# Optimization experiments

Hardware: AMD Instinct MI355X
Metric: run time of the kernel (lower is better)

The kernel has to match this reference:

```python
import jax, jax.numpy as jnp
import numpy as np

SHARPNESS = 2


def setup_inputs() -> dict:
    key = jax.random.key(0)
    k1, k2, k3 = jax.random.split(key, 3)
    x = jax.random.normal(k1, (16, 256, 48, 48), dtype=jnp.float32)
    # 1x1 conv == per-pixel linear: weight (out_c, in_c), bias (out_c,)
    W = jax.random.normal(k2, (256, 256), dtype=jnp.float32) * 0.0625
    bias = jax.random.normal(k3, (256,), dtype=jnp.float32) * 0.01
    return {"x": x, "W": W, "bias": bias}


def reference(x, W, bias):
    b, c, h, w = x.shape
    hw = h * w
    # sample-wide L2 norm over the full (c*h*w) vector (faithful to source)
    xn = jnp.linalg.norm(x.reshape(b, -1), axis=1).reshape(b, 1, 1)
    # NOTE: raw reshapes of the (b,c,h,w)-contiguous tensor, NOT transposes
    x1 = x.reshape(b, hw, c) / xn
    x2 = x.reshape(b, c, hw) / xn
    cos = jnp.einsum('bnc,bcm->bnm', x1, x2)          # (b, hw, hw)
    s = jnp.maximum(cos, 0.0) ** SHARPNESS            # relu^sharpness
    # transform block: 1x1 conv
    tr = jnp.einsum('oc,bchw->bohw', W, x) + bias[None, :, None, None]
    tr = tr.reshape(b, hw, c)                         # raw reshape, as in source
    y = jnp.einsum('bnm,bmc->bnc', s, tr)             # (b, hw, c)
    return y.reshape(b, c, h, w)
```

## Files before the change

### kernel.cpp

```cpp
#include <hip/hip_runtime.h>

#define NB 16
#define NC 256
#define HW 2304
#define CHW 589824

typedef __attribute__((ext_vector_type(8))) short bf16x8;
typedef __attribute__((ext_vector_type(16))) float f32x16;

union BF8 { bf16x8 v; unsigned short u[8]; unsigned d[4]; };

__device__ inline unsigned short f2bf(float f) {
  unsigned u = __builtin_bit_cast(unsigned, f);
  u += 0x7fffu + ((u >> 16) & 1u);
  return (unsigned short)(u >> 16);
}

__device__ inline unsigned f2bf2(float lo, float hi) {
  unsigned r;
  asm("v_cvt_pk_bf16_f32 %0, %1, %2" : "=v"(r) : "v"(lo), "v"(hi));
  return r;
}

__global__ __launch_bounds__(256) void prep_kernel(const float* __restrict__ x,
                                                   const float* __restrict__ W,
                                                   unsigned short* __restrict__ wp,
                                                   unsigned short* __restrict__ xtp,
                                                   double* __restrict__ partials) {
  __shared__ __align__(16) char smem[33344];
  const int bid = blockIdx.x;
  const int tid = threadIdx.x;

  if (bid < 8) {
    const int rt = bid;
    float* tile = (float*)smem;
    const float4* src = (const float4*)(W + (size_t)rt * 32 * 256);
    #pragma unroll
    for (int it = 0; it < 8; ++it) {
      const int i = tid + 256 * it;
      float4 v = src[i];
      const int fi = 4 * i, row = fi >> 8, col = fi & 255;
      *(float4*)&tile[row * 260 + col] = v;
    }
    __syncthreads();
    const int w = tid >> 6, l = tid & 63, l31 = l & 31, h = l >> 5;
    unsigned short* dst = wp + (size_t)rt * 8192;
    #pragma unroll
    for (int ff = 0; ff < 4; ++ff) {
      const int f = 4 * w + ff;
      const float* rp = &tile[l31 * 260 + 16 * f + 8 * h];
      const float4 r0 = *(const float4*)rp;
      const float4 r1 = *(const float4*)(rp + 4);
      BF8 o;
      o.d[0] = f2bf2(r0.x, r0.y);
      o.d[1] = f2bf2(r0.z, r0.w);
      o.d[2] = f2bf2(r1.x, r1.y);
      o.d[3] = f2bf2(r1.z, r1.w);
      *(bf16x8*)(dst + (((size_t)f) * 64 + l) * 8) = o.v;
    }
  } else {
    const int e = bid - 8;
    const int mt = e % 36, kt = (e / 36) % 4, b = e / 144;
    const int m0 = mt * 64, k0 = kt * 64;
    float* tile = (float*)smem;
    double* red = (double*)(smem + 17408);
    const float* xb = x + (size_t)b * CHW;
    double ss = 0.0;
    #pragma unroll
    for (int it = 0; it < 4; ++it) {
      const int i = tid + 256 * it;
      const int row = i >> 4, c4 = (i & 15) * 4;
      float4 v = *(const float4*)(xb + (size_t)(k0 + row) * HW + m0 + c4);
      *(float4*)&tile[row * 68 + c4] = v;
      ss += (double)v.x * v.x + (double)v.y * v.y + (double)v.z * v.z + (double)v.w * v.w;
    }
    #pragma unroll
    for (int off = 32; off > 0; off >>= 1) ss += __shfl_down(ss, off, 64);
    const int w = tid >> 6, l = tid & 63;
    if (l == 0) red[w] = ss;
    __syncthreads();
    if (tid == 0) partials[b * 144 + kt * 36 + mt] = red[0] + red[1] + red[2] + red[3];
    const int l31 = l & 31, h = l >> 5;
    unsigned short* dst = xtp + (size_t)b * CHW;
    #pragma unroll
    for (int pp = 0; pp < 2; ++pp) {
      const int p = 2 * w + pp, mbl = p >> 2, fl = p & 3;
      BF8 o;
      #pragma unroll
      for (int jj = 0; jj < 4; ++jj) {
        const float e0 = tile[(16 * fl + 8 * h + 2 * jj) * 68 + 32 * mbl + l31];
        const float e1 = tile[(16 * fl + 8 * h + 2 * jj + 1) * 68 + 32 * mbl + l31];
        o.d[jj] = f2bf2(e0, e1);
      }
      const int mb = 2 * mt + mbl, f = 4 * kt + fl;
      *(bf16x8*)(dst + (((size_t)mb * 16 + f) * 64 + l) * 8) = o.v;
    }
  }
}

__global__ __launch_bounds__(512, 1) void conv2_kernel(const unsigned short* __restrict__ wp,
                                                       const float* __restrict__ bias,
                                                       const unsigned short* __restrict__ xtp,
                                                       unsigned short* __restrict__ trp,
                                                       const double* __restrict__ partials,
                                                       float* __restrict__ inv_xn2) {
  const int bid = blockIdx.x;
  if (bid == 128) {
    const int t = threadIdx.x;
    if (t >= 256) return;
    const int b = t >> 4, i0 = t & 15;
    double v = 0.0;
    for (int i = i0; i < 144; i += 16) v += partials[b * 144 + i];
    v += __shfl_down(v, 8, 64);
    v += __shfl_down(v, 4, 64);
    v += __shfl_down(v, 2, 64);
    v += __shfl_down(v, 1, 64);
    if (i0 == 0) inv_xn2[b] = (float)(1.0 / v);
    return;
  }
  const int xcd = bid & 7, q = bid >> 3;
  const int b = xcd + 8 * (q & 1);
  const int rt = q >> 1;
  const int tid = threadIdx.x, w = tid >> 6, l = tid & 63, l31 = l & 31, h = l >> 5;
  const unsigned short* xb = xtp + (size_t)b * CHW;

  __shared__ unsigned short tile[32 * 2312];

  bf16x8 af[16];
  #pragma unroll
  for (int f = 0; f < 16; ++f)
    af[f] = *(const bf16x8*)(wp + (((size_t)rt * 16 + f) * 64 + l) * 8);
  float bcol[16];
  #pragma unroll
  for (int reg = 0; reg < 16; ++reg) {
    const int rowl = (reg & 3) + 8 * (reg >> 2) + 4 * h;
    bcol[reg] = bias[32 * rt + rowl];
  }

  for (int i = 0; i < 9; ++i) {
    const int mb = 9 * w + i;
    f32x16 acc;
    #pragma unroll
    for (int r = 0; r < 16; ++r) acc[r] = 0.f;
    #pragma unroll
    for (int f = 0; f < 16; ++f) {
      bf16x8 bv = *(const bf16x8*)(xb + (((size_t)mb * 16 + f) * 64 + l) * 8);
      acc = __builtin_amdgcn_mfma_f32_32x32x16_bf16(af[f], bv, acc, 0, 0, 0);
    }
    #pragma unroll
    for (int p = 0; p < 8; ++p) {
      const int r0 = 2 * p, r1 = 2 * p + 1;
      const int rowl = (r0 & 3) + 8 * (r0 >> 2) + 4 * h;
      const unsigned pk = f2bf2(acc[r0] + bcol[r0], acc[r1] + bcol[r1]);
      tile[rowl * 2312 + mb * 32 + l31] = (unsigned short)pk;
      tile[(rowl + 1) * 2312 + mb * 32 + l31] = (unsigned short)(pk >> 16);
    }
  }
  __syncthreads();

  unsigned short* tb = trp + (size_t)b * CHW;
  for (int si = 0; si < 18; ++si) {
    const int id = 18 * w + si;
    const int kfi = id >> 3, cb8 = id & 7;
    const int mbase = 288 * rt + 16 * kfi;
    const int mb2 = mbase >> 6, kf = (mbase >> 4) & 3;
    BF8 o;
    #pragma unroll
    for (int j = 0; j < 8; ++j) {
      const int m = mbase + 8 * h + j;
      const int a = m / 9, s = m - 9 * a;
      o.u[j] = tile[(a - 32 * rt) * 2312 + 256 * s + 32 * cb8 + l31];
    }
    *(bf16x8*)(tb + (size_t)mb2 * 16384 + (((size_t)cb8 * 4 + kf) * 64 + l) * 8) = o.v;
  }
}

#define CHUNK_BODY(CH, CUR, NXT)                                                                   \
  {                                                                                                \
    const int ch_ = (CH);                                                                          \
    const int pb_ = ch_ & 1;                                                                       \
    f32x16 s0, s1;                                                                                 \
    _Pragma("unroll")                                                                              \
    for (int i = 0; i < 16; ++i) { s0[i] = 0.f; s1[i] = 0.f; }                                     \
    _Pragma("unroll")                                                                              \
    for (int f = 0; f < 16; ++f) {                                                                 \
      bf16x8 a0 = *(const bf16x8*)(Af + f * 512 + lane * 8);                                       \
      bf16x8 a1 = *(const bf16x8*)(Af + (16 + f) * 512 + lane * 8);                                \
      s0 = __builtin_amdgcn_mfma_f32_32x32x16_bf16(a0, CUR[f], s0, 0, 0, 0);                       \
      s1 = __builtin_amdgcn_mfma_f32_32x32x16_bf16(a1, CUR[f], s1, 0, 0, 0);                       \
    }                                                                                              \
    bf16x8 bt0[8], bt1[8];                                                                         \
    _Pragma("unroll")                                                                              \
    for (int kk = 0; kk < 8; ++kk) {                                                               \
      const size_t mb_ = 2 * ch_ + (kk >> 2);                                                      \
      bt0[kk] = *(const bf16x8*)(ttb + mb_ * 16384 + ((size_t)((2 * c) * 4 + (kk & 3))) * 512 + lane * 8);     \
      bt1[kk] = *(const bf16x8*)(ttb + mb_ * 16384 + ((size_t)((2 * c + 1) * 4 + (kk & 3))) * 512 + lane * 8); \
    }                                                                                              \
    _Pragma("unroll")                                                                              \
    for (int reg = 0; reg < 16; ++reg) {                                                           \
      const int rowp = (reg & 3) + 8 * (reg >> 2) + 4 * h;                                         \
      float v0 = fmaxf(s0[reg] * inv2, 0.f); v0 *= v0;                                             \
      float v1 = fmaxf(s1[reg] * inv2, 0.f); v1 *= v1;                                             \
      Pl[pb_][rowp][32 * c + l31] = f2bf(v0);                                                      \
      Pl[pb_][32 + rowp][32 * c + l31] = f2bf(v1);                                                 \
    }                                                                                              \
    const int chn_ = (ch_ < 17) ? ch_ + 1 : 17;                                                    \
    const unsigned short* bpn_ = xtb + (size_t)((4 * chn_ + c) * 16) * 512 + lane * 8;             \
    _Pragma("unroll")                                                                              \
    for (int f = 0; f < 16; ++f) NXT[f] = *(const bf16x8*)(bpn_ + f * 512);                        \
    __syncthreads();                                                                               \
    _Pragma("unroll")                                                                              \
    for (int kk = 0; kk < 8; ++kk) {                                                               \
      bf16x8 pf0 = *(const bf16x8*)&Pl[pb_][l31][16 * kk + 8 * h];                                 \
      bf16x8 pf1 = *(const bf16x8*)&Pl[pb_][32 + l31][16 * kk + 8 * h];                            \
      yacc[0][0] = __builtin_amdgcn_mfma_f32_32x32x16_bf16(pf0, bt0[kk], yacc[0][0], 0, 0, 0);     \
      yacc[1][0] = __builtin_amdgcn_mfma_f32_32x32x16_bf16(pf1, bt0[kk], yacc[1][0], 0, 0, 0);     \
      yacc[0][1] = __builtin_amdgcn_mfma_f32_32x32x16_bf16(pf0, bt1[kk], yacc[0][1], 0, 0, 0);     \
      yacc[1][1] = __builtin_amdgcn_mfma_f32_32x32x16_bf16(pf1, bt1[kk], yacc[1][1], 0, 0, 0);     \
    }                                                                                              \
  }

__global__ __launch_bounds__(256, 2) void fused_kernel(const float* __restrict__ x,
                                                       const unsigned short* __restrict__ xtp,
                                                       const unsigned short* __restrict__ trp,
                                                       const float* __restrict__ inv_xn2,
                                                       float* __restrict__ out) {
  const int bid = blockIdx.x;
  const int xcd = bid & 7, j = bid >> 3;
  const int hi = (j >= 36) ? 1 : 0;
  const int b = xcd + 8 * hi;
  const int nt = j - 36 * hi;
  const float* xsrc = x + (size_t)b * CHW;
  const unsigned short* xtb = xtp + (size_t)b * CHW;
  const unsigned short* ttb = trp + (size_t)b * CHW;
  float* ob = out + (size_t)b * CHW;
  const float inv2 = inv_xn2[b];

  const int tid = threadIdx.x;
  const int c = tid >> 6, lane = tid & 63;
  const int l31 = lane & 31, h = lane >> 5;

  __shared__ unsigned short Af[16384];
  __shared__ unsigned short Pl[2][64][136];

  {
    #pragma unroll
    for (int it = 0; it < 8; ++it) {
      const int idx = tid + 256 * it;
      const int f = idx >> 6, l = idx & 63;
      const int ll31 = l & 31, hh = l >> 5;
      const float* sp = xsrc + (size_t)(64 * nt + 32 * (f >> 4) + ll31) * 256 + 16 * (f & 15) + 8 * hh;
      const float4 r0 = *(const float4*)sp;
      const float4 r1 = *(const float4*)(sp + 4);
      BF8 o;
      o.d[0] = f2bf2(r0.x, r0.y);
      o.d[1] = f2bf2(r0.z, r0.w);
      o.d[2] = f2bf2(r1.x, r1.y);
      o.d[3] = f2bf2(r1.z, r1.w);
      *(bf16x8*)(Af + (size_t)f * 512 + (size_t)l * 8) = o.v;
    }
  }

  bf16x8 bva[16], bvb[16];
  {
    const unsigned short* bp0 = xtb + (size_t)(c * 16) * 512 + lane * 8;
    #pragma unroll
    for (int f = 0; f < 16; ++f) bva[f] = *(const bf16x8*)(bp0 + f * 512);
  }
  __syncthreads();

  f32x16 yacc[2][2];
  #pragma unroll
  for (int nh = 0; nh < 2; ++nh)
    #pragma unroll
    for (int cb = 0; cb < 2; ++cb)
      #pragma unroll
      for (int i = 0; i < 16; ++i) yacc[nh][cb][i] = 0.f;

  for (int ci = 0; ci < 9; ++ci) {
    CHUNK_BODY(2 * ci, bva, bvb)
    CHUNK_BODY(2 * ci + 1, bvb, bva)
  }

  #pragma unroll
  for (int nh = 0; nh < 2; ++nh)
    #pragma unroll
    for (int cb = 0; cb < 2; ++cb) {
      const int col = 64 * c + 32 * cb + l31;
      #pragma unroll
      for (int reg = 0; reg < 16; ++reg) {
        const int rowp = (reg & 3) + 8 * (reg >> 2) + 4 * h;
        ob[(size_t)(64 * nt + 32 * nh + rowp) * NC + col] = yacc[nh][cb][reg];
      }
    }
}

extern "C" void kernel_launch(void* const* d_in, const int* in_sizes, int n_in,
                              void* d_out, int out_size, void* d_ws, size_t ws_size,
                              hipStream_t stream) {
  const float* x    = (const float*)d_in[0];
  const float* W    = (const float*)d_in[1];
  const float* bias = (const float*)d_in[2];
  float* out = (float*)d_out;

  const size_t SZ = (size_t)NB * CHW * sizeof(unsigned short);
  double* partials       = (double*)d_ws;
  float* inv_xn2         = (float*)((char*)d_ws + 24576);
  unsigned short* wp     = (unsigned short*)((char*)d_ws + 32768);
  unsigned short* xtp    = (unsigned short*)((char*)d_ws + 163840 + SZ);
  unsigned short* trp    = (unsigned short*)((char*)d_ws + 163840 + 3 * SZ);

  prep_kernel<<<2312, 256, 0, stream>>>(x, W, wp, xtp, partials);
  conv2_kernel<<<129, 512, 0, stream>>>(wp, bias, xtp, trp, partials, inv_xn2);
  fused_kernel<<<576, 256, 0, stream>>>(x, xtp, trp, inv_xn2, out);
}
```

Before: 232.8 us.

## Split conv kernel into 1025 small blocks over channel-column slices

The 1x1-conv kernel is repartitioned from 128 large 512-thread blocks, each holding a 32x2304 shared tile, to 1024 blocks of 192 threads. Each block handles one cb8 column group across 9 spatial slices, so the shared tile shrinks to 32x296. The aim is to fill more CUs and raise occupancy for a small kernel that was limited to one block per CU. In exchange, each block reloads the same W fragments and bias, which adds redundant weight traffic.

```diff
diff --git a/kernel.cpp b/kernel.cpp
--- a/kernel.cpp
+++ b/kernel.cpp
@@ -98,33 +98,33 @@
   }
 }
 
-__global__ __launch_bounds__(512, 1) void conv2_kernel(const unsigned short* __restrict__ wp,
-                                                       const float* __restrict__ bias,
-                                                       const unsigned short* __restrict__ xtp,
-                                                       unsigned short* __restrict__ trp,
-                                                       const double* __restrict__ partials,
-                                                       float* __restrict__ inv_xn2) {
+__global__ __launch_bounds__(192) void conv3_kernel(const unsigned short* __restrict__ wp,
+                                                    const float* __restrict__ bias,
+                                                    const unsigned short* __restrict__ xtp,
+                                                    unsigned short* __restrict__ trp,
+                                                    const double* __restrict__ partials,
+                                                    float* __restrict__ inv_xn2) {
   const int bid = blockIdx.x;
-  if (bid == 128) {
+  if (bid == 1024) {
     const int t = threadIdx.x;
-    if (t >= 256) return;
-    const int b = t >> 4, i0 = t & 15;
+    if (t >= 128) return;
+    const int b = t >> 3, i0 = t & 7;
     double v = 0.0;
-    for (int i = i0; i < 144; i += 16) v += partials[b * 144 + i];
-    v += __shfl_down(v, 8, 64);
+    for (int i = i0; i < 144; i += 8) v += partials[b * 144 + i];
     v += __shfl_down(v, 4, 64);
     v += __shfl_down(v, 2, 64);
     v += __shfl_down(v, 1, 64);
     if (i0 == 0) inv_xn2[b] = (float)(1.0 / v);
     return;
   }
-  const int xcd = bid & 7, q = bid >> 3;
-  const int b = xcd + 8 * (q & 1);
-  const int rt = q >> 1;
+  const int xcd = bid & 7, r = bid >> 3;
+  const int b = xcd + 8 * (r & 1);
+  const int r2 = r >> 1;
+  const int rt = r2 >> 3, cb8 = r2 & 7;
   const int tid = threadIdx.x, w = tid >> 6, l = tid & 63, l31 = l & 31, h = l >> 5;
   const unsigned short* xb = xtp + (size_t)b * CHW;
 
-  __shared__ unsigned short tile[32 * 2312];
+  __shared__ unsigned short tile[32 * 296];
 
   bf16x8 af[16];
   #pragma unroll
@@ -137,11 +137,13 @@
     bcol[reg] = bias[32 * rt + rowl];
   }
 
-  for (int i = 0; i < 9; ++i) {
-    const int mb = 9 * w + i;
+  #pragma unroll
+  for (int si = 0; si < 3; ++si) {
+    const int s = 3 * w + si;
+    const int mb = 8 * s + cb8;
     f32x16 acc;
     #pragma unroll
-    for (int r = 0; r < 16; ++r) acc[r] = 0.f;
+    for (int rr = 0; rr < 16; ++rr) acc[rr] = 0.f;
     #pragma unroll
     for (int f = 0; f < 16; ++f) {
       bf16x8 bv = *(const bf16x8*)(xb + (((size_t)mb * 16 + f) * 64 + l) * 8);
@@ -152,16 +154,16 @@
       const int r0 = 2 * p, r1 = 2 * p + 1;
       const int rowl = (r0 & 3) + 8 * (r0 >> 2) + 4 * h;
       const unsigned pk = f2bf2(acc[r0] + bcol[r0], acc[r1] + bcol[r1]);
-      tile[rowl * 2312 + mb * 32 + l31] = (unsigned short)pk;
-      tile[(rowl + 1) * 2312 + mb * 32 + l31] = (unsigned short)(pk >> 16);
+      tile[rowl * 296 + 32 * s + l31] = (unsigned short)pk;
+      tile[(rowl + 1) * 296 + 32 * s + l31] = (unsigned short)(pk >> 16);
     }
   }
   __syncthreads();
 
   unsigned short* tb = trp + (size_t)b * CHW;
-  for (int si = 0; si < 18; ++si) {
-    const int id = 18 * w + si;
-    const int kfi = id >> 3, cb8 = id & 7;
+  #pragma unroll
+  for (int si = 0; si < 6; ++si) {
+    const int kfi = 6 * w + si;
     const int mbase = 288 * rt + 16 * kfi;
     const int mb2 = mbase >> 6, kf = (mbase >> 4) & 3;
     BF8 o;
@@ -169,7 +171,7 @@
     for (int j = 0; j < 8; ++j) {
       const int m = mbase + 8 * h + j;
       const int a = m / 9, s = m - 9 * a;
-      o.u[j] = tile[(a - 32 * rt) * 2312 + 256 * s + 32 * cb8 + l31];
+      o.u[j] = tile[(a - 32 * rt) * 296 + 32 * s + l31];
     }
     *(bf16x8*)(tb + (size_t)mb2 * 16384 + (((size_t)cb8 * 4 + kf) * 64 + l) * 8) = o.v;
   }
@@ -311,6 +313,6 @@
   unsigned short* trp    = (unsigned short*)((char*)d_ws + 163840 + 3 * SZ);
 
   prep_kernel<<<2312, 256, 0, stream>>>(x, W, wp, xtp, partials);
-  conv2_kernel<<<129, 512, 0, stream>>>(wp, bias, xtp, trp, partials, inv_xn2);
+  conv3_kernel<<<1025, 192, 0, stream>>>(wp, bias, xtp, trp, partials, inv_xn2);
   fused_kernel<<<576, 256, 0, stream>>>(x, xtp, trp, inv_xn2, out);
 }
```

Measured after the change: 234.2 us. No clear change (+0.6%).
